# Kernel tuning notes

Measured on AMD Instinct MI355X. Metric: run time of the kernel, lower is better.

The kernel has to match this reference:

```python
import jax, jax.numpy as jnp
import numpy as np

EPS = 1e-5


def _conv(x, k, pad):
    # x: (B,C,H,W), k: (Co,Ci,kh,kw)
    return jax.lax.conv_general_dilated(
        x, k, window_strides=(1, 1), padding=pad,
        dimension_numbers=("NCHW", "OIHW", "NCHW"))


def _prop_rows(x, k, b, g, bt, m, v, a, reverse):
    # direction 'D' (reverse=False) or 'U' (reverse=True).
    # conv on a 1xW stripe with 3x3 pad1 only uses the middle kernel row.
    kmid = k[:, :, 1:2, :]  # (C,C,1,3)
    # conv(current + res) = (K*current + b) + K*res ; precompute per-row part.
    pre = _conv(x, kmid, [(0, 0), (1, 1)]) + b[None, :, None, None]  # (B,C,H,W)
    inv = g / jnp.sqrt(v + EPS)
    mn, bn_b = m[None, :, None], bt[None, :, None]
    inv3 = inv[None, :, None]

    def step(res, pre_i):  # res, pre_i: (B,C,W)
        h = pre_i + _conv(res[:, :, None, :], kmid, [(0, 0), (1, 1)])[:, :, 0, :]
        y = (h - mn) * inv3 + bn_b
        y = jnp.where(y >= 0, y, a * y)  # PReLU (single shared param)
        return y, y

    B, _, H, W = x.shape
    res0 = jnp.zeros((B, k.shape[0], W), x.dtype)
    xs = jnp.moveaxis(pre, 2, 0)  # (H,B,C,W)
    _, ys = jax.lax.scan(step, res0, xs, reverse=reverse)
    return jnp.moveaxis(ys, 0, 2)  # (B,C,H,W)


def _prop_cols(x, k, b, g, bt, m, v, a, reverse):
    # direction 'R' (reverse=False) or 'L' (reverse=True); only middle kernel col used.
    kmid = k[:, :, :, 1:2]  # (C,C,3,1)
    pre = _conv(x, kmid, [(1, 1), (0, 0)]) + b[None, :, None, None]  # (B,C,H,W)
    inv = g / jnp.sqrt(v + EPS)
    mn, bn_b = m[None, :, None], bt[None, :, None]
    inv3 = inv[None, :, None]

    def step(res, pre_i):  # res, pre_i: (B,C,H)
        h = pre_i + _conv(res[:, :, :, None], kmid, [(1, 1), (0, 0)])[:, :, :, 0]
        y = (h - mn) * inv3 + bn_b
        y = jnp.where(y >= 0, y, a * y)
        return y, y

    B, _, H, W = x.shape
    res0 = jnp.zeros((B, k.shape[0], H), x.dtype)
    xs = jnp.moveaxis(pre, 3, 0)  # (W,B,C,H)
    _, ys = jax.lax.scan(step, res0, xs, reverse=reverse)
    return jnp.moveaxis(ys, 0, 3)  # (B,C,H,W)


def setup_inputs() -> dict:
    key = jax.random.key(0)
    ks = jax.random.split(key, 16)
    B, C, H, W = 8, 128, 160, 160
    x = jax.random.normal(ks[0], (B, C, H, W), jnp.float32)
    # std ~ 1/sqrt(fan_in=C*3) keeps the recurrence stable
    kernels = jax.random.normal(ks[1], (4, C, C, 3, 3), jnp.float32) * 0.04
    biases = jax.random.normal(ks[2], (4, C), jnp.float32) * 0.05
    bn_gamma = 1.0 + 0.1 * jax.random.normal(ks[3], (4, C), jnp.float32)
    bn_beta = 0.1 * jax.random.normal(ks[4], (4, C), jnp.float32)
    bn_mean = 0.1 * jax.random.normal(ks[5], (4, C), jnp.float32)
    bn_var = 1.0 + 0.1 * jax.random.uniform(ks[6], (4, C), jnp.float32)
    prelu_a = jnp.full((4,), 0.25, jnp.float32)
    fus_w = jax.random.normal(ks[7], (C, 4 * C), jnp.float32) * 0.04
    fus_b = jax.random.normal(ks[8], (C,), jnp.float32) * 0.05
    fbn_gamma = 1.0 + 0.1 * jax.random.normal(ks[9], (C,), jnp.float32)
    fbn_beta = 0.1 * jax.random.normal(ks[10], (C,), jnp.float32)
    fbn_mean = 0.1 * jax.random.normal(ks[11], (C,), jnp.float32)
    fbn_var = 1.0 + 0.1 * jax.random.uniform(ks[12], (C,), jnp.float32)
    return dict(x=x, kernels=kernels, biases=biases, bn_gamma=bn_gamma,
                bn_beta=bn_beta, bn_mean=bn_mean, bn_var=bn_var,
                prelu_a=prelu_a, fus_w=fus_w, fus_b=fus_b,
                fbn_gamma=fbn_gamma, fbn_beta=fbn_beta, fbn_mean=fbn_mean,
                fbn_var=fbn_var)


def reference(x, kernels, biases, bn_gamma, bn_beta, bn_mean, bn_var, prelu_a,
              fus_w, fus_b, fbn_gamma, fbn_beta, fbn_mean, fbn_var):
    def p(i):
        return (kernels[i], biases[i], bn_gamma[i], bn_beta[i], bn_mean[i],
                bn_var[i], prelu_a[i])

    feat_D = _prop_rows(x, *p(0), reverse=False)
    feat_U = _prop_rows(x, *p(1), reverse=True)
    feat_R = _prop_cols(x, *p(2), reverse=False)
    feat_L = _prop_cols(x, *p(3), reverse=True)
    feat = jnp.concatenate([feat_D, feat_U, feat_R, feat_L], axis=1)  # (B,4C,H,W)
    out = jnp.einsum("oc,bchw->bohw", fus_w, feat) + fus_b[None, :, None, None]
    inv = fbn_gamma / jnp.sqrt(fbn_var + EPS)
    out = (out - fbn_mean[None, :, None, None]) * inv[None, :, None, None] \
        + fbn_beta[None, :, None, None]
    return jax.nn.relu(out)
```

## Files before the change

kernel.cpp:

```cpp
#include <hip/hip_runtime.h>
#include <stdint.h>


typedef __attribute__((ext_vector_type(8))) __bf16 bf16x8;
typedef __attribute__((ext_vector_type(4))) float f32x4;

#define DEV static __device__ __forceinline__

DEV unsigned short f2bf(float f) {
  union { float f; unsigned int u; } v; v.f = f;
  unsigned int u = v.u;
  u += 0x7fffu + ((u >> 16) & 1u);
  return (unsigned short)(u >> 16);
}
DEV float bf2f(unsigned short s) {
  union { float f; unsigned int u; } v; v.u = ((unsigned int)s) << 16;
  return v.f;
}
DEV f32x4 mfma16(bf16x8 a, bf16x8 b, f32x4 c) {
  return __builtin_amdgcn_mfma_f32_16x16x32_bf16(a, b, c, 0, 0, 0);
}
DEV void barrier_lds() {
  asm volatile("s_waitcnt lgkmcnt(0)\n\ts_barrier" ::: "memory");
}

constexpr int Hc = 160, Wc = 160, Cc = 128;
constexpr int CHUNK = 32, NCH = 5;
constexpr int SR = 50;
constexpr int SPAD = 136;

constexpr long WS_XT    = 0;
constexpr long WS_WPREP = 104857600;
constexpr long WS_EPI   = 105250816;
constexpr long WS_FWT   = 105254912;
constexpr long WS_FEPI  = 105385984;
constexpr long WS_FEAT  = 105387008;
constexpr long WS_TOTAL = 315102208;
constexpr int EX_WORDS = 160 * 2 * 8 * 128;

__global__ void prep_kernel(const float* __restrict__ kern, const float* __restrict__ bias,
                            const float* __restrict__ bg, const float* __restrict__ bb,
                            const float* __restrict__ bm, const float* __restrict__ bv,
                            const float* __restrict__ fw, const float* __restrict__ fb2,
                            const float* __restrict__ fg, const float* __restrict__ fbt,
                            const float* __restrict__ fm, const float* __restrict__ fv,
                            unsigned short* __restrict__ wprep, float2* __restrict__ epi,
                            unsigned short* __restrict__ fwT, float2* __restrict__ fepi,
                            unsigned int* __restrict__ exz)
{
  int idx = blockIdx.x * 256 + threadIdx.x;
  if (idx < EX_WORDS) exz[idx] = 0;
  if (idx < 196608) {
    int c = idx & 127;
    int t = (idx >> 7) % 3;
    int o = (idx / 384) & 127;
    int d = idx / 49152;
    int kh = (d < 2) ? 1 : t;
    int kw = (d < 2) ? t : 1;
    wprep[idx] = f2bf(kern[(((d * 128 + o) * 128 + c) * 3 + kh) * 3 + kw]);
  }
  int i2 = idx - 196608;
  if (i2 >= 0 && i2 < 65536) fwT[i2] = f2bf(fw[i2]);
  int i3 = idx - 262144;
  if (i3 >= 0 && i3 < 512) {
    float sc = bg[i3] / sqrtf(bv[i3] + 1e-5f);
    epi[i3] = make_float2(sc, (bias[i3] - bm[i3]) * sc + bb[i3]);
  }
  int i4 = idx - 262656;
  if (i4 >= 0 && i4 < 128) {
    float sc = fg[i4] / sqrtf(fv[i4] + 1e-5f);
    fepi[i4] = make_float2(sc, (fb2[i4] - fm[i4]) * sc + fbt[i4]);
  }
}

__global__ void transpose_kernel(const float* __restrict__ x, float* __restrict__ xT)
{
  __shared__ float tile[32][33];
  int b = blockIdx.z, h = blockIdx.y;
  int c0 = (blockIdx.x / 5) * 32, w0 = (blockIdx.x % 5) * 32;
  int tx = threadIdx.x & 31, ty = threadIdx.x >> 5;
#pragma unroll
  for (int r = 0; r < 4; r++) {
    int c = c0 + ty + 8 * r;
    tile[ty + 8 * r][tx] = x[(((long)b * 128 + c) * 160 + h) * 160 + w0 + tx];
  }
  __syncthreads();
#pragma unroll
  for (int r = 0; r < 4; r++) {
    int w = w0 + ty + 8 * r;
    xT[(((long)b * 160 + h) * 160 + w) * 128 + c0 + tx] = tile[tx][ty + 8 * r];
  }
}

#define SCAN_STEP(T, PAR, PUB)                                                  \
  do {                                                                          \
    const int t_ = (T);                                                         \
    const int i_ = rev ? (159 - t_) : t_;                                       \
    const bool last_ = (t_ == 159);                                             \
    const unsigned short* cur_ = sbuf[PAR];                                     \
    unsigned short* nxt_ = sbuf[(PAR) ^ 1];                                     \
               \
    if (!last_) {                                                               \
      const float* xr_ = xb + (long)(rev ? (i_ - 1) : (i_ + 1)) * si;           \
      _Pragma("unroll") for (int m = 0; m < 3; m++)                             \
        _Pragma("unroll") for (int r = 0; r < 4; r++)                           \
          xn[m][r] = xr_[xoff[m][r]];                                           \
    }                                                                           \
           \
    f32x4 acc[3];                                                               \
    acc[0] = (f32x4){0.f, 0.f, 0.f, 0.f};                                       \
    acc[1] = (f32x4){0.f, 0.f, 0.f, 0.f};                                       \
    acc[2] = (f32x4){0.f, 0.f, 0.f, 0.f};                                       \
    _Pragma("unroll") for (int kt = 0; kt < 12; kt++) {                         \
      const int tt_ = kt >> 2;                                                  \
      const int cc_ = ((kt & 3) << 5) + (kq << 3);                              \
      _Pragma("unroll") for (int m = 0; m < 3; m++) {                           \
        const bf16x8 A_ = *(const bf16x8*)&cur_[(m * 16 + ncol + tt_) * SPAD + cc_]; \
        acc[m] = mfma16(A_, Bfrag[kt], acc[m]);                                 \
      }                                                                         \
    }                                                                           \
                                                 \
    _Pragma("unroll") for (int m = 0; m < 3; m++)                               \
      _Pragma("unroll") for (int r = 0; r < 4; r++) {                           \
        float v_ = acc[m][r] * ep.x + ep.y;                                     \
        v_ = (v_ >= 0.f) ? v_ : (aslope * v_);                                  \
        yf[m][r] = v_; yb[m][r] = f2bf(v_);                                     \
      }                                                                         \
                      \
    if (PUB) {                                                                  \
      const unsigned int tagv_ = ((unsigned int)((t_ + 1) >> 3)) << 16;         \
      _Pragma("unroll") for (int r = 0; r < 4; r++) {                           \
        const unsigned int pv_ = (kq >= 2) ? (unsigned int)yb[0][r]             \
                                           : (unsigned int)yb[2][r];            \
        __hip_atomic_store(pubp + r * 128, tagv_ | pv_,                         \
                           __ATOMIC_RELAXED, __HIP_MEMORY_SCOPE_AGENT);         \
      }                                                                         \
    }                                                                           \
               \
    if (!last_) {                                                               \
      _Pragma("unroll") for (int m = 0; m < 3; m++)                             \
        _Pragma("unroll") for (int r = 0; r < 4; r++) {                         \
          unsigned short sv_ = 0;                                               \
          if (xok[m][r]) sv_ = f2bf(xn[m][r] + yf[m][r]);                       \
          nxt_[(m * 16 + kq * 4 + r + 1) * SPAD + o] = sv_;                     \
        }                                                                       \
    }                                                                           \
                             \
    {                                                                           \
      unsigned short* frow_ = fbp + (long)i_ * fi;                              \
      _Pragma("unroll") for (int r = 0; r < 4; r++) {                           \
        frow_[foff0[r]] = yb[1][r];                                             \
        frow_[foff1[r]] = (kq >= 2) ? yb[0][r] : yb[2][r];                      \
      }                                                                         \
    }                                                                           \
    barrier_lds();                                                              \
  } while (0)

#define EXCH_FILL(T, PARN)                                                      \
  do {                                                                          \
    const int tn_ = (T) + 1;                                                    \
    const unsigned int e_ = (unsigned int)(tn_ >> 3);                           \
    const int in_ = rev ? (159 - tn_) : tn_;                                    \
    unsigned short* nxt_ = sbuf[PARN];                                          \
    const float* xr_ = xb + (long)in_ * si;                                     \
    _Pragma("unroll") for (int k = 0; k < 4; k++) {                             \
      const int c_ = tid + (k << 9);                                            \
      const int side_ = c_ >> 10;                                               \
      const int rr_ = (c_ >> 7) & 7;                                            \
      const int ch_ = c_ & 127;                                                 \
      const int u_ = side_ ? (u0 + 32 + rr_) : (u0 - 8 + rr_);                  \
      const int lsp_ = side_ ? (41 + rr_) : (rr_ + 1);                          \
      unsigned short sv_ = 0;                                                   \
      if (u_ >= 0 && u_ < 160) {                                                \
        const unsigned int* slot_ = exbase +                                    \
            (long)(side_ ? (sid + 1) : (sid - 1)) * 2048 +                      \
            (((side_ ^ 1) << 3) + rr_) * 128 + ch_;                             \
        const float xv_ = xr_[u_ * su + ch_];                                   \
        unsigned int v_ = __hip_atomic_load(slot_, __ATOMIC_RELAXED,            \
                                            __HIP_MEMORY_SCOPE_AGENT);          \
        while ((v_ >> 16) != e_) {                                              \
          __builtin_amdgcn_s_sleep(1);                                          \
          v_ = __hip_atomic_load(slot_, __ATOMIC_RELAXED,                       \
                                 __HIP_MEMORY_SCOPE_AGENT);                     \
        }                                                                       \
        sv_ = f2bf(xv_ + bf2f((unsigned short)(v_ & 0xffffu)));                 \
      }                                                                         \
      nxt_[lsp_ * SPAD + ch_] = sv_;                                            \
    }                                                                           \
    barrier_lds();                                                              \
  } while (0)

__global__ __launch_bounds__(512, 1) void scan_kernel(
    const float* __restrict__ xT, const unsigned short* __restrict__ wprep,
    const float2* __restrict__ epi, const float* __restrict__ prelu_a,
    unsigned short* __restrict__ featbuf, unsigned int* exbase)
{
  __shared__ __align__(16) unsigned short sbuf[2][SR * SPAD];

  const int bid = blockIdx.x;
  const int q = bid >> 5;
  const int g = bid & 31;
  const int d = g >> 3;
  const int b = g & 7;
  const int tid = threadIdx.x;
  const int wv = tid >> 6;
  const int lane = tid & 63;
  const int ncol = lane & 15;
  const int kq = lane >> 4;
  const int o = wv * 16 + ncol;
  const bool rev = (d & 1);
  const int u0 = q * CHUNK;

  const bool row_mode = (d < 2);
  const long si = row_mode ? (long)Wc * Cc : (long)Cc;
  const int  su = row_mode ? Cc : Wc * Cc;
  const long fi = row_mode ? (long)Wc * 512 : (long)512;
  const int  fu = row_mode ? 512 : Wc * 512;
  const float* xb = xT + (long)b * Hc * Wc * Cc;
  unsigned short* fbp = featbuf + (long)b * Hc * Wc * 512 + d * 128;

  bf16x8 Bfrag[12];
  {
    const unsigned short* wp = wprep + ((long)(d * 128 + o)) * 384;
#pragma unroll
    for (int kt = 0; kt < 12; kt++)
      Bfrag[kt] = *(const bf16x8*)(wp + kt * 32 + kq * 8);
  }
  const float2 ep = epi[d * 128 + o];
  const float aslope = prelu_a[d];

  int xoff[3][4]; bool xok[3][4];
#pragma unroll
  for (int m = 0; m < 3; m++)
#pragma unroll
    for (int r = 0; r < 4; r++) {
      const int u = u0 - 8 + m * 16 + kq * 4 + r;
      const bool ok = (u >= 0 && u < 160);
      xok[m][r] = ok;
      xoff[m][r] = (ok ? u : 0) * su + o;
    }
  int foff0[4], foff1[4];
#pragma unroll
  for (int r = 0; r < 4; r++) {
    foff0[r] = (u0 + 8 + kq * 4 + r) * fu + o;
    const int u1 = (kq >= 2) ? (u0 + (kq - 2) * 4 + r)
                             : (u0 + 24 + kq * 4 + r);
    foff1[r] = u1 * fu + o;
  }

  const int sid = d * 40 + b * 5 + q;
  unsigned int* exw = exbase + (long)sid * 2048;
  unsigned int* pubp = exw + (((kq >= 2) ? (0 * 8 + (kq - 2) * 4)
                                         : (1 * 8 + kq * 4)) * 128 + o);

  const int i0 = rev ? (Hc - 1) : 0;
  for (int e = tid; e < SR * 64; e += 512) {
    const int lsp = e >> 6, cp = e & 63;
    const int u = u0 - 9 + lsp;
    unsigned int sv = 0;
    if (u >= 0 && u < 160) {
      const float2 xv2 = *(const float2*)(xb + (long)i0 * si + (long)u * su + cp * 2);
      sv = (unsigned int)f2bf(xv2.x) | ((unsigned int)f2bf(xv2.y) << 16);
    }
    *(unsigned int*)&sbuf[0][lsp * SPAD + cp * 2] = sv;
  }
  barrier_lds();

  float yf[3][4]; unsigned short yb[3][4]; float xn[3][4];

#pragma unroll 1
  for (int t = 0; t < 160; t += 2) {
    SCAN_STEP(t, 0, false);
    const bool ex = ((t & 7) == 6) && (t != 158);
    SCAN_STEP(t + 1, 1, ex);
    if (ex) EXCH_FILL(t + 1, 0);
  }
}
#undef SCAN_STEP
#undef EXCH_FILL

__global__ __launch_bounds__(256, 1) void fusion_kernel(
    const unsigned short* __restrict__ featbuf, const unsigned short* __restrict__ fwT,
    const float2* __restrict__ fepi, float* __restrict__ out)
{
  __shared__ unsigned short At[32 * 520];
  const int bx = blockIdx.x;
  const int b = bx / 800, mb = bx - b * 800;
  const long m0 = (long)mb * 32;
  const int tid = threadIdx.x, lane = tid & 63, wv = tid >> 6;
  const int ncol = lane & 15, kq = lane >> 4;

  const unsigned short* fp = featbuf + ((long)b * 25600 + m0) * 512;
#pragma unroll
  for (int rr = 0; rr < 8; rr++) {
    const int e = tid + rr * 256;
    const int m = e >> 6, kp = e & 63;
    *(bf16x8*)&At[m * 520 + kp * 8] = *(const bf16x8*)(fp + (long)m * 512 + kp * 8);
  }
  bf16x8 Bf[2][16];
  float2 fe[2];
#pragma unroll
  for (int j = 0; j < 2; j++) {
    const int o = (wv * 2 + j) * 16 + ncol;
    const unsigned short* wp = fwT + (long)o * 512;
#pragma unroll
    for (int kt = 0; kt < 16; kt++)
      Bf[j][kt] = *(const bf16x8*)(wp + kt * 32 + kq * 8);
    fe[j] = fepi[o];
  }
  __syncthreads();

  f32x4 acc[2][2];
#pragma unroll
  for (int mt = 0; mt < 2; mt++)
#pragma unroll
    for (int j = 0; j < 2; j++)
      acc[mt][j] = (f32x4){0.f, 0.f, 0.f, 0.f};
#pragma unroll
  for (int kt = 0; kt < 16; kt++) {
    const bf16x8 A0 = *(const bf16x8*)&At[ncol * 520 + kt * 32 + kq * 8];
    const bf16x8 A1 = *(const bf16x8*)&At[(16 + ncol) * 520 + kt * 32 + kq * 8];
    acc[0][0] = mfma16(A0, Bf[0][kt], acc[0][0]);
    acc[0][1] = mfma16(A0, Bf[1][kt], acc[0][1]);
    acc[1][0] = mfma16(A1, Bf[0][kt], acc[1][0]);
    acc[1][1] = mfma16(A1, Bf[1][kt], acc[1][1]);
  }
#pragma unroll
  for (int mt = 0; mt < 2; mt++)
#pragma unroll
    for (int j = 0; j < 2; j++) {
      const int o = (wv * 2 + j) * 16 + ncol;
      const long hw = m0 + mt * 16 + kq * 4;
      f32x4 v;
#pragma unroll
      for (int r = 0; r < 4; r++) {
        const float z = acc[mt][j][r] * fe[j].x + fe[j].y;
        v[r] = (z > 0.f) ? z : 0.f;
      }
      *(f32x4*)(out + ((long)(b * 128 + o)) * 25600 + hw) = v;
    }
}

extern "C" void kernel_launch(void* const* d_in, const int* in_sizes, int n_in,
                              void* d_out, int out_size, void* d_ws, size_t ws_size,
                              hipStream_t stream)
{
  if (ws_size < (size_t)WS_TOTAL) return;

  const float* x        = (const float*)d_in[0];
  const float* kernels  = (const float*)d_in[1];
  const float* biases   = (const float*)d_in[2];
  const float* bn_gamma = (const float*)d_in[3];
  const float* bn_beta  = (const float*)d_in[4];
  const float* bn_mean  = (const float*)d_in[5];
  const float* bn_var   = (const float*)d_in[6];
  const float* prelu_a  = (const float*)d_in[7];
  const float* fus_w    = (const float*)d_in[8];
  const float* fus_b    = (const float*)d_in[9];
  const float* fbn_g    = (const float*)d_in[10];
  const float* fbn_b    = (const float*)d_in[11];
  const float* fbn_m    = (const float*)d_in[12];
  const float* fbn_v    = (const float*)d_in[13];

  char* ws = (char*)d_ws;
  float*          xT      = (float*)(ws + WS_XT);
  unsigned short* wprep   = (unsigned short*)(ws + WS_WPREP);
  float2*         epi     = (float2*)(ws + WS_EPI);
  unsigned short* fwT     = (unsigned short*)(ws + WS_FWT);
  float2*         fepi    = (float2*)(ws + WS_FEPI);
  unsigned short* featbuf = (unsigned short*)(ws + WS_FEAT);
  unsigned int*   ex      = (unsigned int*)d_out;
  float*          out     = (float*)d_out;

  prep_kernel<<<1280, 256, 0, stream>>>(kernels, biases, bn_gamma, bn_beta, bn_mean, bn_var,
                                        fus_w, fus_b, fbn_g, fbn_b, fbn_m, fbn_v,
                                        wprep, epi, fwT, fepi, ex);
  transpose_kernel<<<dim3(20, 160, 8), 256, 0, stream>>>(x, xT);
  scan_kernel<<<160, 512, 0, stream>>>(xT, wprep, epi, prelu_a, featbuf, ex);
  fusion_kernel<<<6400, 256, 0, stream>>>(featbuf, fwT, fepi, out);
}
```

Before: 651.8 us.

## Split scan into 8 chunks of 20 with halo 6 across 256 blocks

```diff
diff --git a/kernel.cpp b/kernel.cpp
--- a/kernel.cpp
+++ b/kernel.cpp
@@ -25,8 +25,9 @@
 }
 
 constexpr int Hc = 160, Wc = 160, Cc = 128;
-constexpr int CHUNK = 32, NCH = 5;
-constexpr int SR = 50;
+constexpr int CHUNK = 20, NCH = 8;
+constexpr int HALO = 6;
+constexpr int SR = 34;
 constexpr int SPAD = 136;
 
 constexpr long WS_XT    = 0;
@@ -36,7 +37,8 @@
 constexpr long WS_FEPI  = 105385984;
 constexpr long WS_FEAT  = 105387008;
 constexpr long WS_TOTAL = 315102208;
-constexpr int EX_WORDS = 160 * 2 * 8 * 128;
+constexpr int EX_STRIDE = 2 * 6 * 128;
+constexpr int EX_WORDS  = 256 * EX_STRIDE;
 
 __global__ void prep_kernel(const float* __restrict__ kern, const float* __restrict__ bias,
                             const float* __restrict__ bg, const float* __restrict__ bb,
@@ -99,86 +101,84 @@
     const bool last_ = (t_ == 159);                                             \
     const unsigned short* cur_ = sbuf[PAR];                                     \
     unsigned short* nxt_ = sbuf[(PAR) ^ 1];                                     \
-               \
+              \
     if (!last_) {                                                               \
       const float* xr_ = xb + (long)(rev ? (i_ - 1) : (i_ + 1)) * si;           \
-      _Pragma("unroll") for (int m = 0; m < 3; m++)                             \
+      _Pragma("unroll") for (int j = 0; j < 2; j++)                             \
         _Pragma("unroll") for (int r = 0; r < 4; r++)                           \
-          xn[m][r] = xr_[xoff[m][r]];                                           \
-    }                                                                           \
-           \
-    f32x4 acc[3];                                                               \
-    acc[0] = (f32x4){0.f, 0.f, 0.f, 0.f};                                       \
-    acc[1] = (f32x4){0.f, 0.f, 0.f, 0.f};                                       \
-    acc[2] = (f32x4){0.f, 0.f, 0.f, 0.f};                                       \
+          xn[j][r] = xr_[xoff[r] + 16 * j];                                     \
+    }                                                                           \
+               \
+    f32x4 acc0_ = {0.f, 0.f, 0.f, 0.f}, acc1_ = {0.f, 0.f, 0.f, 0.f};           \
     _Pragma("unroll") for (int kt = 0; kt < 12; kt++) {                         \
       const int tt_ = kt >> 2;                                                  \
       const int cc_ = ((kt & 3) << 5) + (kq << 3);                              \
-      _Pragma("unroll") for (int m = 0; m < 3; m++) {                           \
-        const bf16x8 A_ = *(const bf16x8*)&cur_[(m * 16 + ncol + tt_) * SPAD + cc_]; \
-        acc[m] = mfma16(A_, Bfrag[kt], acc[m]);                                 \
-      }                                                                         \
+      const bf16x8 A_ = *(const bf16x8*)&cur_[(m * 16 + ncol + tt_) * SPAD + cc_]; \
+      acc0_ = mfma16(A_, Bfrag[0][kt], acc0_);                                  \
+      acc1_ = mfma16(A_, Bfrag[1][kt], acc1_);                                  \
     }                                                                           \
                                                  \
-    _Pragma("unroll") for (int m = 0; m < 3; m++)                               \
-      _Pragma("unroll") for (int r = 0; r < 4; r++) {                           \
-        float v_ = acc[m][r] * ep.x + ep.y;                                     \
-        v_ = (v_ >= 0.f) ? v_ : (aslope * v_);                                  \
-        yf[m][r] = v_; yb[m][r] = f2bf(v_);                                     \
-      }                                                                         \
+    _Pragma("unroll") for (int r = 0; r < 4; r++) {                             \
+      float v0_ = acc0_[r] * ep[0].x + ep[0].y;                                 \
+      v0_ = (v0_ >= 0.f) ? v0_ : (aslope * v0_);                                \
+      yf[0][r] = v0_; yb[0][r] = f2bf(v0_);                                     \
+      float v1_ = acc1_[r] * ep[1].x + ep[1].y;                                 \
+      v1_ = (v1_ >= 0.f) ? v1_ : (aslope * v1_);                                \
+      yf[1][r] = v1_; yb[1][r] = f2bf(v1_);                                     \
+    }                                                                           \
                       \
     if (PUB) {                                                                  \
-      const unsigned int tagv_ = ((unsigned int)((t_ + 1) >> 3)) << 16;         \
-      _Pragma("unroll") for (int r = 0; r < 4; r++) {                           \
-        const unsigned int pv_ = (kq >= 2) ? (unsigned int)yb[0][r]             \
-                                           : (unsigned int)yb[2][r];            \
-        __hip_atomic_store(pubp + r * 128, tagv_ | pv_,                         \
-                           __ATOMIC_RELAXED, __HIP_MEMORY_SCOPE_AGENT);         \
-      }                                                                         \
-    }                                                                           \
-               \
+      const unsigned int tagv_ = ((unsigned int)exidx) << 16;                   \
+      _Pragma("unroll") for (int r = 0; r < 4; r++)                             \
+        if (pok[r]) {                                                           \
+          __hip_atomic_store(exw + pubidx[r], tagv_ | (unsigned int)yb[0][r],   \
+                             __ATOMIC_RELAXED, __HIP_MEMORY_SCOPE_AGENT);       \
+          __hip_atomic_store(exw + pubidx[r] + 16, tagv_ | (unsigned int)yb[1][r], \
+                             __ATOMIC_RELAXED, __HIP_MEMORY_SCOPE_AGENT);       \
+        }                                                                       \
+    }                                                                           \
+             \
     if (!last_) {                                                               \
-      _Pragma("unroll") for (int m = 0; m < 3; m++)                             \
+      _Pragma("unroll") for (int j = 0; j < 2; j++)                             \
         _Pragma("unroll") for (int r = 0; r < 4; r++) {                         \
           unsigned short sv_ = 0;                                               \
-          if (xok[m][r]) sv_ = f2bf(xn[m][r] + yf[m][r]);                       \
-          nxt_[(m * 16 + kq * 4 + r + 1) * SPAD + o] = sv_;                     \
+          if (xok[r]) sv_ = f2bf(xn[j][r] + yf[j][r]);                          \
+          nxt_[(m * 16 + kq * 4 + r + 1) * SPAD + o0 + 16 * j] = sv_;           \
         }                                                                       \
     }                                                                           \
-                             \
+                     \
     {                                                                           \
       unsigned short* frow_ = fbp + (long)i_ * fi;                              \
-      _Pragma("unroll") for (int r = 0; r < 4; r++) {                           \
-        frow_[foff0[r]] = yb[1][r];                                             \
-        frow_[foff1[r]] = (kq >= 2) ? yb[0][r] : yb[2][r];                      \
-      }                                                                         \
+      _Pragma("unroll") for (int j = 0; j < 2; j++)                             \
+        _Pragma("unroll") for (int r = 0; r < 4; r++)                           \
+          if (fok[r]) frow_[foff[r] + 16 * j] = yb[j][r];                       \
     }                                                                           \
     barrier_lds();                                                              \
   } while (0)
 
-#define EXCH_FILL(T, PARN)                                                      \
+#define EXCH_FILL(T)                                                            \
   do {                                                                          \
     const int tn_ = (T) + 1;                                                    \
-    const unsigned int e_ = (unsigned int)(tn_ >> 3);                           \
     const int in_ = rev ? (159 - tn_) : tn_;                                    \
-    unsigned short* nxt_ = sbuf[PARN];                                          \
+    unsigned short* nxt_ = sbuf[0];    \
     const float* xr_ = xb + (long)in_ * si;                                     \
-    _Pragma("unroll") for (int k = 0; k < 4; k++) {                             \
-      const int c_ = tid + (k << 9);                                            \
-      const int side_ = c_ >> 10;                                               \
-      const int rr_ = (c_ >> 7) & 7;                                            \
-      const int ch_ = c_ & 127;                                                 \
-      const int u_ = side_ ? (u0 + 32 + rr_) : (u0 - 8 + rr_);                  \
-      const int lsp_ = side_ ? (41 + rr_) : (rr_ + 1);                          \
+    _Pragma("unroll") for (int k = 0; k < 3; k++) {                             \
+      const int c_ = tid + (k << 9);                  \
+      const int side_ = (c_ >= 768);                                            \
+      const int idx_ = side_ ? (c_ - 768) : c_;                                 \
+      const int rr_ = idx_ >> 7;                                                \
+      const int ch_ = idx_ & 127;                                               \
+      const int u_ = side_ ? (u0 + 20 + rr_) : (u0 - 6 + rr_);                  \
+      const int lsp_ = side_ ? (27 + rr_) : (1 + rr_);                          \
       unsigned short sv_ = 0;                                                   \
       if (u_ >= 0 && u_ < 160) {                                                \
         const unsigned int* slot_ = exbase +                                    \
-            (long)(side_ ? (sid + 1) : (sid - 1)) * 2048 +                      \
-            (((side_ ^ 1) << 3) + rr_) * 128 + ch_;                             \
+            (long)(side_ ? (sid + 1) : (sid - 1)) * EX_STRIDE +                 \
+            (((side_ ^ 1) * 6) + rr_) * 128 + ch_;                              \
         const float xv_ = xr_[u_ * su + ch_];                                   \
         unsigned int v_ = __hip_atomic_load(slot_, __ATOMIC_RELAXED,            \
                                             __HIP_MEMORY_SCOPE_AGENT);          \
-        while ((v_ >> 16) != e_) {                                              \
+        while ((v_ >> 16) != (unsigned int)exidx) {                             \
           __builtin_amdgcn_s_sleep(1);                                          \
           v_ = __hip_atomic_load(slot_, __ATOMIC_RELAXED,                       \
                                  __HIP_MEMORY_SCOPE_AGENT);                     \
@@ -187,6 +187,7 @@
       }                                                                         \
       nxt_[lsp_ * SPAD + ch_] = sv_;                                            \
     }                                                                           \
+    exidx++;                                                                    \
     barrier_lds();                                                              \
   } while (0)
 
@@ -204,10 +205,12 @@
   const int b = g & 7;
   const int tid = threadIdx.x;
   const int wv = tid >> 6;
+  const int m = wv >> 2;
+  const int ng = wv & 3;
   const int lane = tid & 63;
   const int ncol = lane & 15;
   const int kq = lane >> 4;
-  const int o = wv * 16 + ncol;
+  const int o0 = ng * 32 + ncol;
   const bool rev = (d & 1);
   const int u0 = q * CHUNK;
 
@@ -219,44 +222,42 @@
   const float* xb = xT + (long)b * Hc * Wc * Cc;
   unsigned short* fbp = featbuf + (long)b * Hc * Wc * 512 + d * 128;
 
-  bf16x8 Bfrag[12];
-  {
+  bf16x8 Bfrag[2][12];
+  float2 ep[2];
+#pragma unroll
+  for (int j = 0; j < 2; j++) {
+    const int o = o0 + 16 * j;
     const unsigned short* wp = wprep + ((long)(d * 128 + o)) * 384;
 #pragma unroll
     for (int kt = 0; kt < 12; kt++)
-      Bfrag[kt] = *(const bf16x8*)(wp + kt * 32 + kq * 8);
-  }
-  const float2 ep = epi[d * 128 + o];
+      Bfrag[j][kt] = *(const bf16x8*)(wp + kt * 32 + kq * 8);
+    ep[j] = epi[d * 128 + o];
+  }
   const float aslope = prelu_a[d];
 
-  int xoff[3][4]; bool xok[3][4];
-#pragma unroll
-  for (int m = 0; m < 3; m++)
-#pragma unroll
-    for (int r = 0; r < 4; r++) {
-      const int u = u0 - 8 + m * 16 + kq * 4 + r;
-      const bool ok = (u >= 0 && u < 160);
-      xok[m][r] = ok;
-      xoff[m][r] = (ok ? u : 0) * su + o;
-    }
-  int foff0[4], foff1[4];
+  int xoff[4]; bool xok[4];
+  int foff[4]; bool fok[4];
+  int pubidx[4]; bool pok[4];
 #pragma unroll
   for (int r = 0; r < 4; r++) {
-    foff0[r] = (u0 + 8 + kq * 4 + r) * fu + o;
-    const int u1 = (kq >= 2) ? (u0 + (kq - 2) * 4 + r)
-                             : (u0 + 24 + kq * 4 + r);
-    foff1[r] = u1 * fu + o;
-  }
-
-  const int sid = d * 40 + b * 5 + q;
-  unsigned int* exw = exbase + (long)sid * 2048;
-  unsigned int* pubp = exw + (((kq >= 2) ? (0 * 8 + (kq - 2) * 4)
-                                         : (1 * 8 + kq * 4)) * 128 + o);
+    const int ext = m * 16 + kq * 4 + r;
+    const int u = u0 - 6 + ext;
+    xok[r] = (u >= 0 && u < 160);
+    xoff[r] = (xok[r] ? u : 0) * su + o0;
+    fok[r] = (ext >= 6 && ext < 26);
+    foff[r] = (fok[r] ? u : 0) * fu + o0;
+    if (ext >= 6 && ext < 12)       { pok[r] = true;  pubidx[r] = (ext - 6) * 128 + o0; }
+    else if (ext >= 20 && ext < 26) { pok[r] = true;  pubidx[r] = (6 + ext - 20) * 128 + o0; }
+    else                            { pok[r] = false; pubidx[r] = 0; }
+  }
+
+  const int sid = (d * 8 + b) * 8 + q;
+  unsigned int* exw = exbase + (long)sid * EX_STRIDE;
 
   const int i0 = rev ? (Hc - 1) : 0;
   for (int e = tid; e < SR * 64; e += 512) {
     const int lsp = e >> 6, cp = e & 63;
-    const int u = u0 - 9 + lsp;
+    const int u = u0 - 7 + lsp;
     unsigned int sv = 0;
     if (u >= 0 && u < 160) {
       const float2 xv2 = *(const float2*)(xb + (long)i0 * si + (long)u * su + cp * 2);
@@ -266,14 +267,15 @@
   }
   barrier_lds();
 
-  float yf[3][4]; unsigned short yb[3][4]; float xn[3][4];
+  float yf[2][4]; unsigned short yb[2][4]; float xn[2][4];
+  int exidx = 1;
 
 #pragma unroll 1
-  for (int t = 0; t < 160; t += 2) {
-    SCAN_STEP(t, 0, false);
-    const bool ex = ((t & 7) == 6) && (t != 158);
-    SCAN_STEP(t + 1, 1, ex);
-    if (ex) EXCH_FILL(t + 1, 0);
+  for (int tb = 0; tb < 160; tb += 2) {
+    SCAN_STEP(tb, 0, false);
+    const bool ex = (((tb + 1) % 6) == 5);
+    SCAN_STEP(tb + 1, 1, ex);
+    if (ex) EXCH_FILL(tb + 1);
   }
 }
 #undef SCAN_STEP
@@ -372,10 +374,10 @@
   unsigned int*   ex      = (unsigned int*)d_out;
   float*          out     = (float*)d_out;
 
-  prep_kernel<<<1280, 256, 0, stream>>>(kernels, biases, bn_gamma, bn_beta, bn_mean, bn_var,
+  prep_kernel<<<1536, 256, 0, stream>>>(kernels, biases, bn_gamma, bn_beta, bn_mean, bn_var,
                                         fus_w, fus_b, fbn_g, fbn_b, fbn_m, fbn_v,
                                         wprep, epi, fwT, fepi, ex);
   transpose_kernel<<<dim3(20, 160, 8), 256, 0, stream>>>(x, xT);
-  scan_kernel<<<160, 512, 0, stream>>>(xT, wprep, epi, prelu_a, featbuf, ex);
+  scan_kernel<<<256, 512, 0, stream>>>(xT, wprep, epi, prelu_a, featbuf, ex);
   fusion_kernel<<<6400, 256, 0, stream>>>(featbuf, fwT, fepi, out);
 }
```

Measured after the change: 568.5 us. 1.15x faster.
